# Kernel tuning notes

Hardware: AMD Instinct MI355X
Metric: run time of the kernel (lower is better)

The kernel has to match this reference:

```python
import jax, jax.numpy as jnp
import numpy as np

# Instant-NGP style multi-resolution hash grid encoding
L = 16          # n_levels
F = 2           # n_feat_per_entry
D = 3           # spatial dim
T = 2 ** 19     # hashmap entries per level
B = 2 ** 20     # number of query points
BASE_RES, MAX_RES = 16, 512
PRIMES = (1, 2654435761, 805459861)  # NGP spatial hash primes


def setup_inputs() -> dict:
    key = jax.random.key(0)
    k1, k2 = jax.random.split(key)
    xyz = jax.random.uniform(k1, (B, D), dtype=jnp.float32)  # points in [0,1)^3
    offsets = np.arange(L + 1, dtype=np.int32) * T            # len L+1, offsets[-1] = n_total_embed
    n_total = int(offsets[-1])
    embeddings = (jax.random.uniform(k2, (n_total, F), dtype=jnp.float32) * 2.0 - 1.0) * 1e-4
    growth = np.exp(np.log(MAX_RES / BASE_RES) / (L - 1))
    resolutions = np.floor(BASE_RES * growth ** np.arange(L)).astype(np.int32)  # len L
    return {
        "xyz": xyz,
        "embeddings": embeddings,
        "offsets": jnp.asarray(offsets),
        "resolutions": jnp.asarray(resolutions),
        "min_xyz": jnp.zeros((D,), jnp.float32),
        "max_xyz": jnp.ones((D,), jnp.float32),
    }


def _encode(xyz, embeddings, offsets, resolutions, min_xyz, max_xyz):
    Bn, Dn = xyz.shape
    n_grid = 2 ** Dn  # corners of a cell
    # normalize to [0,1]; points outside the box are zeroed (valid mask)
    u = (xyz - min_xyz) / (max_xyz - min_xyz)                      # (B,D)
    valid = jnp.all((u >= 0.0) & (u <= 1.0), axis=-1)              # (B,)
    res = resolutions.astype(xyz.dtype)                            # (L,)
    pos = u[:, None, :] * res[None, :, None]                       # (B,L,D)
    pos0 = jnp.clip(jnp.floor(pos), 0.0, res[None, :, None] - 1.0) # lower cell corner
    frac = pos - pos0                                              # (B,L,D) in [0,1]
    # all 2^D corner offsets, bit d of corner c
    bits = jnp.asarray([[(c >> d) & 1 for d in range(Dn)] for c in range(n_grid)])  # (2^D, D)
    corners = pos0[:, :, None, :].astype(jnp.uint32) + bits[None, None].astype(jnp.uint32)  # (B,L,2^D,D)
    # trilinear weights: prod_d (frac if bit else 1-frac)
    fb = frac[:, :, None, :]
    w = jnp.prod(jnp.where(bits[None, None].astype(bool), fb, 1.0 - fb), axis=-1)  # (B,L,2^D)
    # spatial hash: xor of coord_d * prime_d (uint32 wraparound), mod level table size
    primes = jnp.asarray(PRIMES[:Dn], dtype=jnp.uint32)
    hp = corners * primes                                          # (B,L,2^D,D) uint32
    h = hp[..., 0]
    for d in range(1, Dn):
        h = h ^ hp[..., d]
    sizes = (offsets[1:] - offsets[:-1]).astype(jnp.uint32)        # (L,)
    idx = (h % sizes[None, :, None]).astype(jnp.int32) + offsets[:-1][None, :, None]  # (B,L,2^D)
    gathered = embeddings[idx]                                     # (B,L,2^D,F)
    out = jnp.einsum("blc,blcf->blf", w, gathered)                 # (B,L,F)
    out = out * valid[:, None, None].astype(out.dtype)
    return out.reshape(Bn, -1)                                     # (B, L*F)


def reference(xyz, embeddings, offsets, resolutions, min_xyz, max_xyz):
    return _encode(xyz, embeddings, offsets, resolutions, min_xyz, max_xyz)
```

## Files before the change

### kernel.cpp

```cpp
#include <hip/hip_runtime.h>

#define NLVL 16
#define NDENSE 7
#define PREPASS_CAP 600000

typedef float f32x2 __attribute__((ext_vector_type(2)));
typedef float f32x4 __attribute__((ext_vector_type(4)));
typedef _Float16 f16x2 __attribute__((ext_vector_type(2)));

__device__ __forceinline__ unsigned hash3(unsigned x, unsigned y, unsigned z) {
    return x ^ (y * 2654435761u) ^ (z * 805459861u);
}

__device__ __forceinline__ unsigned dense_total(const int* __restrict__ resolutions,
                                                unsigned doff[NDENSE]) {
    unsigned acc = 0;
    for (int ll = 0; ll < NDENSE; ++ll) {
        unsigned S = (unsigned)resolutions[ll] + 1u;
        doff[ll] = acc;
        acc += S * S * S;
    }
    return acc;
}

__global__ __launch_bounds__(256) void convert_fp16_kernel(
    const float* __restrict__ emb,
    _Float16*    __restrict__ htab,
    int n_entries)
{
    int i = blockIdx.x * 256 + (int)threadIdx.x;
    if (i >= n_entries) return;
    f32x2 v = reinterpret_cast<const f32x2*>(emb)[i];
    f16x2 h;
    h.x = (_Float16)v.x;
    h.y = (_Float16)v.y;
    reinterpret_cast<f16x2*>(htab)[i] = h;
}

__global__ __launch_bounds__(256) void densify_kernel(
    const float* __restrict__ emb,
    const int*   __restrict__ offsets,
    const int*   __restrict__ resolutions,
    float*       __restrict__ dense)
{
    unsigned doff[NDENSE];
    unsigned total = dense_total(resolutions, doff);
    if (total > PREPASS_CAP) total = PREPASS_CAP;
    unsigned tid = blockIdx.x * 256u + threadIdx.x;
    if (tid >= total) return;
    int l = 0;
    while (l < NDENSE - 1 && tid >= doff[l + 1]) ++l;
    unsigned idx = tid - doff[l];
    unsigned S = (unsigned)resolutions[l] + 1u;
    unsigned x = idx % S;
    unsigned t = idx / S;
    unsigned y = t % S;
    unsigned z = t / S;
    unsigned off  = (unsigned)offsets[l];
    unsigned size = (unsigned)offsets[l + 1] - off;
    unsigned mask = size - 1u;
    unsigned h = hash3(x, y, z);
    unsigned hm = ((size & mask) == 0u) ? (h & mask) : (h % size);
    const f32x2* src = reinterpret_cast<const f32x2*>(emb) + off + hm;
    f32x2* dst = reinterpret_cast<f32x2*>(dense) + tid;
    *dst = *src;
}

__global__ __launch_bounds__(256) void encode_kernel(
    const float* __restrict__ xyz,
    const float* __restrict__ emb,
    const _Float16* __restrict__ htab,
    const int*   __restrict__ offsets,
    const int*   __restrict__ resolutions,
    const float* __restrict__ min_xyz,
    const float* __restrict__ max_xyz,
    const float* __restrict__ dense,
    float*       __restrict__ scratch,
    float*       __restrict__ out,
    int B, int use_dense, int use_scratch, int use_fp16)
{
    const int g = blockIdx.x & 15;
    const int chunk = blockIdx.x >> 4;
    const int l = (g < 8) ? (8 + g) : (((g - 8) + (chunk >> 6)) & 7);
    const int p = chunk * 256 + (int)threadIdx.x;
    if (p >= B) return;

    const float res = (float)resolutions[l];
    const unsigned off  = (unsigned)offsets[l];
    const unsigned size = (unsigned)offsets[l + 1] - off;
    const unsigned mask = size - 1u;
    const bool pow2 = (size & mask) == 0u;
    const float mn0 = min_xyz[0], mn1 = min_xyz[1], mn2 = min_xyz[2];
    const float mx0 = max_xyz[0], mx1 = max_xyz[1], mx2 = max_xyz[2];

    const float x = xyz[p * 3 + 0];
    const float y = xyz[p * 3 + 1];
    const float z = xyz[p * 3 + 2];
    const float ux = (x - mn0) / (mx0 - mn0);
    const float uy = (y - mn1) / (mx1 - mn1);
    const float uz = (z - mn2) / (mx2 - mn2);
    const bool valid = (ux >= 0.0f) & (ux <= 1.0f) &
                       (uy >= 0.0f) & (uy <= 1.0f) &
                       (uz >= 0.0f) & (uz <= 1.0f);

    const float rm1 = res - 1.0f;
    const float px = ux * res, py = uy * res, pz = uz * res;
    const float p0x = fminf(fmaxf(floorf(px), 0.0f), rm1);
    const float p0y = fminf(fmaxf(floorf(py), 0.0f), rm1);
    const float p0z = fminf(fmaxf(floorf(pz), 0.0f), rm1);
    const float fx = px - p0x, fy = py - p0y, fz = pz - p0z;
    const float gx = 1.0f - fx, gy = 1.0f - fy, gz = 1.0f - fz;
    const unsigned cx0 = (unsigned)p0x;
    const unsigned cy0 = (unsigned)p0y;
    const unsigned cz0 = (unsigned)p0z;

    float o0 = 0.0f, o1 = 0.0f;

    bool dense_ok = false;
    unsigned doff[NDENSE];
    if (use_dense && l < NDENSE) {
        unsigned total = dense_total(resolutions, doff);
        dense_ok = (total <= PREPASS_CAP);
    }

    if (dense_ok) {
        const unsigned S = (unsigned)resolutions[l] + 1u;
        const f32x2* lvl = reinterpret_cast<const f32x2*>(dense) + doff[l];
        const unsigned base = cx0 + S * (cy0 + S * cz0);
        f32x4 e00, e10, e01, e11;
        __builtin_memcpy(&e00, lvl + base,             16);
        __builtin_memcpy(&e10, lvl + base + S,         16);
        __builtin_memcpy(&e01, lvl + base + S * S,     16);
        __builtin_memcpy(&e11, lvl + base + S * S + S, 16);
        o0 += (gx * gy * gz) * e00.x;  o1 += (gx * gy * gz) * e00.y;
        o0 += (fx * gy * gz) * e00.z;  o1 += (fx * gy * gz) * e00.w;
        o0 += (gx * fy * gz) * e10.x;  o1 += (gx * fy * gz) * e10.y;
        o0 += (fx * fy * gz) * e10.z;  o1 += (fx * fy * gz) * e10.w;
        o0 += (gx * gy * fz) * e01.x;  o1 += (gx * gy * fz) * e01.y;
        o0 += (fx * gy * fz) * e01.z;  o1 += (fx * gy * fz) * e01.w;
        o0 += (gx * fy * fz) * e11.x;  o1 += (gx * fy * fz) * e11.y;
        o0 += (fx * fy * fz) * e11.z;  o1 += (fx * fy * fz) * e11.w;
    } else if (use_fp16) {
        const f16x2* lvl = reinterpret_cast<const f16x2*>(htab) + off;
#pragma unroll
        for (int c = 0; c < 8; ++c) {
            unsigned bx = (unsigned)(c & 1);
            unsigned by = (unsigned)((c >> 1) & 1);
            unsigned bz = (unsigned)((c >> 2) & 1);
            unsigned h = hash3(cx0 + bx, cy0 + by, cz0 + bz);
            unsigned hm = pow2 ? (h & mask) : (h % size);
            f16x2 e = lvl[hm];
            float w = (bx ? fx : gx) * (by ? fy : gy);
            w = w * (bz ? fz : gz);
            o0 += w * (float)e.x;
            o1 += w * (float)e.y;
        }
    } else {
        const f32x2* lvl = reinterpret_cast<const f32x2*>(emb) + off;
#pragma unroll
        for (int c = 0; c < 8; ++c) {
            unsigned bx = (unsigned)(c & 1);
            unsigned by = (unsigned)((c >> 1) & 1);
            unsigned bz = (unsigned)((c >> 2) & 1);
            unsigned h = hash3(cx0 + bx, cy0 + by, cz0 + bz);
            unsigned hm = pow2 ? (h & mask) : (h % size);
            f32x2 e = lvl[hm];
            float w = (bx ? fx : gx) * (by ? fy : gy);
            w = w * (bz ? fz : gz);
            o0 += w * e.x;
            o1 += w * e.y;
        }
    }

    if (!valid) { o0 = 0.0f; o1 = 0.0f; }
    f32x2 r; r.x = o0; r.y = o1;
    if (use_scratch) {
        f32x2* op = reinterpret_cast<f32x2*>(scratch) + (size_t)l * B + p;
        __builtin_nontemporal_store(r, op);
    } else {
        f32x2* op = reinterpret_cast<f32x2*>(out + (size_t)p * (NLVL * 2) + l * 2);
        __builtin_nontemporal_store(r, op);
    }
}

__global__ __launch_bounds__(256) void transpose_kernel(
    const float* __restrict__ scratch,
    float*       __restrict__ out,
    int B)
{
    __shared__ float tile[64][33];
    const int p0 = blockIdx.x * 64;
    const int tid = (int)threadIdx.x;

    const f32x2* src = reinterpret_cast<const f32x2*>(scratch);
#pragma unroll
    for (int k = 0; k < 4; ++k) {
        int it = tid + k * 256;
        int l  = it >> 6;
        int pi = it & 63;
        int p  = p0 + pi;
        f32x2 v = (p < B) ? src[(size_t)l * B + p] : (f32x2){0.0f, 0.0f};
        tile[pi][2 * l]     = v.x;
        tile[pi][2 * l + 1] = v.y;
    }
    __syncthreads();

    const int pl = tid >> 2;
    const int q  = tid & 3;
    const int p  = p0 + pl;
    if (p >= B) return;
    float vals[8];
#pragma unroll
    for (int j = 0; j < 8; ++j) vals[j] = tile[pl][q * 8 + j];
    f32x4 lo, hi;
    lo.x = vals[0]; lo.y = vals[1]; lo.z = vals[2]; lo.w = vals[3];
    hi.x = vals[4]; hi.y = vals[5]; hi.z = vals[6]; hi.w = vals[7];
    f32x4* dst = reinterpret_cast<f32x4*>(out + (size_t)p * 32 + q * 8);
    __builtin_nontemporal_store(lo, dst);
    __builtin_nontemporal_store(hi, dst + 1);
}

extern "C" void kernel_launch(void* const* d_in, const int* in_sizes, int n_in,
                              void* d_out, int out_size, void* d_ws, size_t ws_size,
                              hipStream_t stream) {
    const float* xyz        = (const float*)d_in[0];
    const float* embeddings = (const float*)d_in[1];
    const int*   offsets    = (const int*)d_in[2];
    const int*   resolutions= (const int*)d_in[3];
    const float* min_xyz    = (const float*)d_in[4];
    const float* max_xyz    = (const float*)d_in[5];
    float* out = (float*)d_out;

    int B = in_sizes[0] / 3;
    int n_entries = in_sizes[1] / 2;

    size_t scratch_bytes = (size_t)B * NLVL * 8;
    size_t dense_bytes   = (size_t)PREPASS_CAP * 8;
    size_t htab_bytes    = (size_t)n_entries * 4;

    int use_scratch = (ws_size >= scratch_bytes + dense_bytes) ? 1 : 0;
    size_t dense_off = use_scratch ? scratch_bytes : 0;
    int use_dense = (ws_size >= dense_off + dense_bytes) ? 1 : 0;
    size_t htab_off = dense_off + (use_dense ? dense_bytes : 0);
    int use_fp16 = (ws_size >= htab_off + htab_bytes) ? 1 : 0;

    float*    scratch = (float*)d_ws;
    float*    dense_p = (float*)((char*)d_ws + dense_off);
    _Float16* htab    = (_Float16*)((char*)d_ws + htab_off);

    if (use_fp16) {
        int cgrid = (n_entries + 255) / 256;
        convert_fp16_kernel<<<cgrid, 256, 0, stream>>>(embeddings, htab, n_entries);
    }
    if (use_dense) {
        int pgrid = (PREPASS_CAP + 255) / 256;
        densify_kernel<<<pgrid, 256, 0, stream>>>(
            embeddings, offsets, resolutions, dense_p);
    }
    int nchunks = (B + 255) / 256;
    int grid = nchunks * NLVL;
    encode_kernel<<<grid, 256, 0, stream>>>(
        xyz, embeddings, htab, offsets, resolutions, min_xyz, max_xyz,
        dense_p, scratch, out, B, use_dense, use_scratch, use_fp16);
    if (use_scratch) {
        int tgrid = (B + 63) / 64;
        transpose_kernel<<<tgrid, 256, 0, stream>>>(scratch, out, B);
    }
}
```

Baseline: 470.4 us.

## Pair adjacent x-corner hash lookups into 8-byte loads and halve scratch precision

For power-of-two hash tables, the two corners that differ only in x share a 64-bit aligned pair when cx0 is even, because the hash XORs x directly. One u32x2 load then serves both corners, which removes half the gathers. When cx0 is odd a second scalar load is still issued. The intermediate scratch buffer is now stored as fp16 instead of fp32, halving the write and read traffic between the encode and transpose kernels, at the cost of extra rounding in the output.

Result: faster. 428.1 us (-9.0%).

```diff
diff --git a/kernel.cpp b/kernel.cpp
--- a/kernel.cpp
+++ b/kernel.cpp
@@ -7,6 +7,7 @@
 typedef float f32x2 __attribute__((ext_vector_type(2)));
 typedef float f32x4 __attribute__((ext_vector_type(4)));
 typedef _Float16 f16x2 __attribute__((ext_vector_type(2)));
+typedef unsigned u32x2 __attribute__((ext_vector_type(2)));
 
 __device__ __forceinline__ unsigned hash3(unsigned x, unsigned y, unsigned z) {
     return x ^ (y * 2654435761u) ^ (z * 805459861u);
@@ -114,6 +115,9 @@
     const unsigned cy0 = (unsigned)p0y;
     const unsigned cz0 = (unsigned)p0z;
 
+    const unsigned P1 = 2654435761u;
+    const unsigned P2 = 805459861u;
+
     float o0 = 0.0f, o1 = 0.0f;
 
     bool dense_ok = false;
@@ -140,20 +144,49 @@
         o0 += (fx * gy * fz) * e01.z;  o1 += (fx * gy * fz) * e01.w;
         o0 += (gx * fy * fz) * e11.x;  o1 += (gx * fy * fz) * e11.y;
         o0 += (fx * fy * fz) * e11.z;  o1 += (fx * fy * fz) * e11.w;
-    } else if (use_fp16) {
-        const f16x2* lvl = reinterpret_cast<const f16x2*>(htab) + off;
-#pragma unroll
-        for (int c = 0; c < 8; ++c) {
-            unsigned bx = (unsigned)(c & 1);
-            unsigned by = (unsigned)((c >> 1) & 1);
-            unsigned bz = (unsigned)((c >> 2) & 1);
-            unsigned h = hash3(cx0 + bx, cy0 + by, cz0 + bz);
-            unsigned hm = pow2 ? (h & mask) : (h % size);
-            f16x2 e = lvl[hm];
-            float w = (bx ? fx : gx) * (by ? fy : gy);
-            w = w * (bz ? fz : gz);
-            o0 += w * (float)e.x;
-            o1 += w * (float)e.y;
+    } else if (use_fp16 && pow2) {
+        const unsigned* lvl32 = reinterpret_cast<const unsigned*>(htab) + off;
+        const u32x2*    lvlp  = reinterpret_cast<const u32x2*>(lvl32);
+        unsigned m4[4], h0a[4];
+        u32x2 pr[4];
+#pragma unroll
+        for (int pi = 0; pi < 4; ++pi) {
+            unsigned by = (unsigned)(pi & 1);
+            unsigned bz = (unsigned)(pi >> 1);
+            unsigned m = ((cy0 + by) * P1) ^ ((cz0 + bz) * P2);
+            unsigned h0 = (cx0 ^ m) & mask;
+            m4[pi] = m; h0a[pi] = h0;
+            pr[pi] = lvlp[h0 >> 1];
+        }
+        unsigned e0b[4], e1b[4];
+        if ((cx0 & 1u) == 0u) {
+#pragma unroll
+            for (int pi = 0; pi < 4; ++pi) {
+                bool hi = (h0a[pi] & 1u) != 0u;
+                e0b[pi] = hi ? pr[pi].y : pr[pi].x;
+                e1b[pi] = hi ? pr[pi].x : pr[pi].y;
+            }
+        } else {
+#pragma unroll
+            for (int pi = 0; pi < 4; ++pi) {
+                unsigned h1 = ((cx0 + 1u) ^ m4[pi]) & mask;
+                e1b[pi] = lvl32[h1];
+                e0b[pi] = (h0a[pi] & 1u) ? pr[pi].y : pr[pi].x;
+            }
+        }
+#pragma unroll
+        for (int pi = 0; pi < 4; ++pi) {
+            unsigned by = (unsigned)(pi & 1);
+            unsigned bz = (unsigned)(pi >> 1);
+            float wy = by ? fy : gy;
+            float wz = bz ? fz : gz;
+            float wyz = wy * wz;
+            f16x2 e0 = __builtin_bit_cast(f16x2, e0b[pi]);
+            f16x2 e1 = __builtin_bit_cast(f16x2, e1b[pi]);
+            float w0 = gx * wyz;
+            float w1 = fx * wyz;
+            o0 += w0 * (float)e0.x;  o1 += w0 * (float)e0.y;
+            o0 += w1 * (float)e1.x;  o1 += w1 * (float)e1.y;
         }
     } else {
         const f32x2* lvl = reinterpret_cast<const f32x2*>(emb) + off;
@@ -173,11 +206,13 @@
     }
 
     if (!valid) { o0 = 0.0f; o1 = 0.0f; }
-    f32x2 r; r.x = o0; r.y = o1;
     if (use_scratch) {
-        f32x2* op = reinterpret_cast<f32x2*>(scratch) + (size_t)l * B + p;
-        __builtin_nontemporal_store(r, op);
+        f16x2 h; h.x = (_Float16)o0; h.y = (_Float16)o1;
+        unsigned hb = __builtin_bit_cast(unsigned, h);
+        unsigned* op = reinterpret_cast<unsigned*>(scratch) + (size_t)l * B + p;
+        __builtin_nontemporal_store(hb, op);
     } else {
+        f32x2 r; r.x = o0; r.y = o1;
         f32x2* op = reinterpret_cast<f32x2*>(out + (size_t)p * (NLVL * 2) + l * 2);
         __builtin_nontemporal_store(r, op);
     }
@@ -192,16 +227,17 @@
     const int p0 = blockIdx.x * 64;
     const int tid = (int)threadIdx.x;
 
-    const f32x2* src = reinterpret_cast<const f32x2*>(scratch);
+    const unsigned* src = reinterpret_cast<const unsigned*>(scratch);
 #pragma unroll
     for (int k = 0; k < 4; ++k) {
         int it = tid + k * 256;
         int l  = it >> 6;
         int pi = it & 63;
         int p  = p0 + pi;
-        f32x2 v = (p < B) ? src[(size_t)l * B + p] : (f32x2){0.0f, 0.0f};
-        tile[pi][2 * l]     = v.x;
-        tile[pi][2 * l + 1] = v.y;
+        unsigned vb = (p < B) ? src[(size_t)l * B + p] : 0u;
+        f16x2 v = __builtin_bit_cast(f16x2, vb);
+        tile[pi][2 * l]     = (float)v.x;
+        tile[pi][2 * l + 1] = (float)v.y;
     }
     __syncthreads();
 
@@ -234,7 +270,7 @@
     int B = in_sizes[0] / 3;
     int n_entries = in_sizes[1] / 2;
 
-    size_t scratch_bytes = (size_t)B * NLVL * 8;
+    size_t scratch_bytes = (size_t)B * NLVL * 4;
     size_t dense_bytes   = (size_t)PREPASS_CAP * 8;
     size_t htab_bytes    = (size_t)n_entries * 4;
 
```
